# Kernel optimization log

Hardware: AMD Instinct MI355X
Metric: run time of the kernel (lower is better)

The kernel has to match this reference:

```python
import jax, jax.numpy as jnp
import numpy as np

DIM = 64  # per-head feature dim used for the 1/sqrt(dim) scale


def setup_inputs() -> dict:
    key = jax.random.key(0)
    kq, kk, kv, kw, kb = jax.random.split(key, 5)
    B, S, D, DK = 32, 4096, 64, 256
    q = jax.random.normal(kq, (B, S, D), dtype=jnp.float32)
    k = jax.random.normal(kk, (B, S, D), dtype=jnp.float32)
    v = jax.random.normal(kv, (B, S, D), dtype=jnp.float32)
    # Linear(input_size=S -> dim_k=DK): weight [DK, S], bias [DK]
    E_w = jax.random.normal(kw, (DK, S), dtype=jnp.float32) * (1.0 / np.sqrt(S))
    E_b = jax.random.normal(kb, (DK,), dtype=jnp.float32) * 0.01
    return {"q": q, "k": k, "v": v, "E_w": E_w, "E_b": E_b}


def reference(q, k, v, E_w, E_b):
    # K projection: k.transpose(1,2) -> [b, d, s]; E(k) -> [b, d, dim_k]
    K = jnp.einsum('bsd,ks->bdk', k, E_w) + E_b  # [b, d, dim_k]
    # scores = q @ K / sqrt(dim) -> [b, s, dim_k]
    scores = jnp.matmul(q, K) / jnp.sqrt(jnp.asarray(DIM, q.dtype))
    P_bar = jax.nn.softmax(scores, axis=-1)  # softmax over projected dim_k axis
    # V projection with F = E (parameter sharing): v -> [b, d, dim_k] -> transpose -> [b, dim_k, d]
    V = jnp.einsum('bsd,ks->bkd', v, E_w) + E_b[None, :, None]  # [b, dim_k, d]
    out = jnp.matmul(P_bar, V)  # [b, s, d]
    return out
```

## Files before the change

### kernel.cpp

```cpp
#include <hip/hip_runtime.h>
#include <hip/hip_bf16.h>
#include <stdint.h>

#define B_  32
#define S_  4096
#define D_  64
#define DK_ 256

typedef float f32x4 __attribute__((ext_vector_type(4)));
typedef short s16x8 __attribute__((ext_vector_type(8)));
typedef uint32_t u32x4 __attribute__((ext_vector_type(4)));

static __device__ __forceinline__ uint16_t f2bf(float f) {
    union { float f; uint32_t u; } x; x.f = f;
    uint32_t u = x.u;
    u += 0x7FFFu + ((u >> 16) & 1u);
    return (uint16_t)(u >> 16);
}

static __device__ __forceinline__ float bf2f(uint32_t hi16) {
    union { uint32_t u; float f; } x; x.u = hi16;
    return x.f;
}

static __device__ __forceinline__ uint32_t pk2(float a, float b) {
    __hip_bfloat162 h = __float22bfloat162_rn(float2{a, b});
    union { __hip_bfloat162 h; uint32_t u; } c; c.h = h;
    return c.u;
}

static __device__ __forceinline__ void gload_lds16(const uint16_t* g, uint16_t* l) {
    __builtin_amdgcn_global_load_lds(
        (const __attribute__((address_space(1))) uint32_t*)g,
        (__attribute__((address_space(3))) uint32_t*)l, 16, 0, 0);
}

__global__ __launch_bounds__(256) void ewcvt(const float* __restrict__ E_w,
                                             uint16_t* __restrict__ EwbS) {
    const int tg     = blockIdx.x * 256 + threadIdx.x;
    const int l16    = tg & 15;
    const int grp    = (tg >> 4) & 3;
    const int schunk = (tg >> 6) & 127;
    const int kktile = tg >> 13;
    const int kk = kktile*16 + l16;
    const int s  = schunk*32 + grp*8;
    const float4 f0 = *(const float4*)(E_w + (size_t)kk * S_ + s);
    const float4 f1 = *(const float4*)(E_w + (size_t)kk * S_ + s + 4);
    s16x8 o;
    o[0] = (short)f2bf(f0.x); o[1] = (short)f2bf(f0.y);
    o[2] = (short)f2bf(f0.z); o[3] = (short)f2bf(f0.w);
    o[4] = (short)f2bf(f1.x); o[5] = (short)f2bf(f1.y);
    o[6] = (short)f2bf(f1.z); o[7] = (short)f2bf(f1.w);
    *(s16x8*)(EwbS + (size_t)tg * 8) = o;
}

__global__ __launch_bounds__(256, 4) void proj_mfma(
        const uint16_t* __restrict__ EwbS,
        const float* __restrict__ kin, const float* __restrict__ vin,
        uint32_t* __restrict__ part) {
    const int bid = blockIdx.x;
    const int ss = bid & 15;
    const int b  = (bid >> 4) & 31;
    const int p  = bid >> 9;
    const float* x = (p ? vin : kin) + (size_t)b * S_ * D_;
    uint32_t* outp = part + ((size_t)((p*32 + b)*16 + ss)) * 8192;

    __shared__ __align__(16) uint16_t lds0[20 * 512];
    __shared__ __align__(16) uint16_t lds1[20 * 512];

    const int tid  = threadIdx.x;
    const int w    = tid >> 6;
    const int lane = tid & 63;
    const int l16  = lane & 15;
    const int grp  = lane >> 4;

    const uint16_t* srcA[4];
    #pragma unroll
    for (int i = 0; i < 4; ++i)
        srcA[i] = EwbS + ((((size_t)(w*4 + i))*128 + ss*8) << 9) + lane*8;

    const int dcol = tid & 63;
    const float* srcB = x + ((size_t)(ss*256 + w*8)) * D_ + dcol;
    const int boff = 16*512 + (dcol >> 4)*512 + (w*16 + (dcol & 15))*8;

    f32x4 acc[4][4] = {};

    {
        float xv[8];
        #pragma unroll
        for (int i = 0; i < 8; ++i) xv[i] = srcB[i * D_];
        #pragma unroll
        for (int i = 0; i < 4; ++i)
            gload_lds16(srcA[i], &lds0[(w*4 + i) * 512]);
        s16x8 h;
        #pragma unroll
        for (int i = 0; i < 8; ++i) h[i] = (short)f2bf(xv[i]);
        *(s16x8*)&lds0[boff] = h;
    }
    __syncthreads();

    #pragma unroll
    for (int t = 0; t < 8; ++t) {
        uint16_t* cur = (t & 1) ? lds1 : lds0;
        uint16_t* nxt = (t & 1) ? lds0 : lds1;

        float xv[8];
        if (t + 1 < 8) {
            const float* sB = srcB + (size_t)(t+1)*32*D_;
            #pragma unroll
            for (int i = 0; i < 8; ++i) xv[i] = sB[i * D_];
            #pragma unroll
            for (int i = 0; i < 4; ++i)
                gload_lds16(srcA[i] + (t+1)*512, &nxt[(w*4 + i) * 512]);
        }

        s16x8 bf[4];
        #pragma unroll
        for (int nt = 0; nt < 4; ++nt)
            bf[nt] = *(const s16x8*)&cur[(16 + nt) * 512 + lane*8];
        #pragma unroll
        for (int m = 0; m < 4; ++m) {
            const s16x8 af = *(const s16x8*)&cur[(w*4 + m) * 512 + lane*8];
            #pragma unroll
            for (int nt = 0; nt < 4; ++nt)
                acc[m][nt] = __builtin_amdgcn_mfma_f32_16x16x32_bf16(af, bf[nt], acc[m][nt], 0, 0, 0);
        }

        if (t + 1 < 8) {
            s16x8 h;
            #pragma unroll
            for (int i = 0; i < 8; ++i) h[i] = (short)f2bf(xv[i]);
            *(s16x8*)&nxt[boff] = h;
        }
        __syncthreads();
    }

    #pragma unroll
    for (int m = 0; m < 4; ++m) {
        const int kkrow = w*64 + m*16 + grp*4;
        #pragma unroll
        for (int nt = 0; nt < 4; ++nt) {
            const int didx = nt*16 + l16;
            outp[didx*128 + (kkrow >> 1)]     = pk2(acc[m][nt][0], acc[m][nt][1]);
            outp[didx*128 + (kkrow >> 1) + 1] = pk2(acc[m][nt][2], acc[m][nt][3]);
        }
    }
}

__global__ __launch_bounds__(256) void bias_reduce(
        const uint32_t* __restrict__ part, const float* __restrict__ E_b,
        uint16_t* __restrict__ Kbf, uint16_t* __restrict__ Vbf) {
    const int b  = blockIdx.x >> 2;
    const int dt = blockIdx.x & 3;
    const int t  = threadIdx.x;

    __shared__ uint16_t Kt[256][18];

    const uint32_t* Kp = part + ((size_t)(b*16))      * 8192 + dt*16*128;
    const uint32_t* Vp = part + ((size_t)((32+b)*16)) * 8192 + dt*16*128;

    #pragma unroll
    for (int j = 0; j < 8; ++j) {
        const int idx = j*256 + t;
        const int d_l = idx >> 7;
        const int kkp = idx & 127;
        float k0 = 0.f, k1 = 0.f, v0 = 0.f, v1 = 0.f;
        #pragma unroll
        for (int s = 0; s < 16; ++s) {
            const uint32_t ku = Kp[(size_t)s*8192 + d_l*128 + kkp];
            const uint32_t vu = Vp[(size_t)s*8192 + d_l*128 + kkp];
            k0 += bf2f(ku << 16);
            k1 += bf2f(ku & 0xffff0000u);
            v0 += bf2f(vu << 16);
            v1 += bf2f(vu & 0xffff0000u);
        }
        const int kk0 = kkp*2;
        const float b0 = E_b[kk0], b1 = E_b[kk0 + 1];
        *(uint32_t*)(Vbf + ((size_t)(b*64 + dt*16 + d_l))*256 + kk0) =
            (uint32_t)f2bf(v0 + b0) | ((uint32_t)f2bf(v1 + b1) << 16);
        Kt[kk0][d_l]     = f2bf(k0 + b0);
        Kt[kk0 + 1][d_l] = f2bf(k1 + b1);
    }
    __syncthreads();

    uint16_t* kout = Kbf + ((size_t)(b*256 + t))*64 + dt*16;
    s16x8 o0, o1;
    #pragma unroll
    for (int i = 0; i < 8; ++i) {
        o0[i] = (short)Kt[t][i];
        o1[i] = (short)Kt[t][8 + i];
    }
    *(s16x8*)kout       = o0;
    *(s16x8*)(kout + 8) = o1;
}

__global__ __launch_bounds__(512, 4) void attn(
        const float* __restrict__ q,
        const uint16_t* __restrict__ Kbf, const uint16_t* __restrict__ Vbf,
        float* __restrict__ out) {
    const int wg   = blockIdx.x;
    const int st   = wg & 31;
    const int b    = wg >> 5;
    const int tid  = threadIdx.x;
    const int wave = tid >> 6;
    const int lane = tid & 63;
    const int l16  = lane & 15;
    const int grp  = lane >> 4;
    const int s0   = st * 128 + wave * 16;

    __shared__ __align__(16) uint16_t Klds[16384];
    __shared__ __align__(16) uint16_t Vlds[16384];

    const uint16_t* Kb = Kbf + (size_t)b * DK_ * D_;
    const uint16_t* Vb = Vbf + (size_t)b * D_ * DK_;

    #pragma unroll
    for (int i = 0; i < 4; ++i) {
        const int s  = wave*4 + i;
        const int nt = s >> 1, kt = s & 1;
        gload_lds16(Kb + (size_t)(nt*16 + l16) * D_ + kt*32 + grp*8, &Klds[s*512]);
    }
    #pragma unroll
    for (int i = 0; i < 4; ++i) {
        const int s   = wave*4 + i;
        const int kt2 = s >> 2, nt2 = s & 3;
        gload_lds16(Vb + (size_t)(nt2*16 + l16) * DK_ + kt2*32 + grp*8, &Vlds[s*512]);
    }

    s16x8 qb[2];
    {
        const float* qp = q + ((size_t)b * S_ + s0 + l16) * D_;
        #pragma unroll
        for (int kt = 0; kt < 2; ++kt) {
            const int d0 = kt*32 + grp*8;
            const float4 f0 = *(const float4*)(qp + d0);
            const float4 f1 = *(const float4*)(qp + d0 + 4);
            s16x8 a;
            a[0] = (short)f2bf(f0.x * 0.125f);
            a[1] = (short)f2bf(f0.y * 0.125f);
            a[2] = (short)f2bf(f0.z * 0.125f);
            a[3] = (short)f2bf(f0.w * 0.125f);
            a[4] = (short)f2bf(f1.x * 0.125f);
            a[5] = (short)f2bf(f1.y * 0.125f);
            a[6] = (short)f2bf(f1.z * 0.125f);
            a[7] = (short)f2bf(f1.w * 0.125f);
            qb[kt] = a;
        }
    }

    __syncthreads();

    f32x4 acc[16] = {};
    #pragma unroll
    for (int nt = 0; nt < 16; ++nt) {
        #pragma unroll
        for (int kt = 0; kt < 2; ++kt) {
            const s16x8 kf = *(const s16x8*)&Klds[(nt*2 + kt)*512 + lane*8];
            acc[nt] = __builtin_amdgcn_mfma_f32_16x16x32_bf16(kf, qb[kt], acc[nt], 0, 0, 0);
        }
    }

    float sm = 0.f;
    #pragma unroll
    for (int nt = 0; nt < 16; ++nt) {
        #pragma unroll
        for (int r = 0; r < 4; ++r) {
            const float e = __expf(acc[nt][r]);
            acc[nt][r] = e;
            sm += e;
        }
    }
    sm += __shfl_xor(sm, 16);
    sm += __shfl_xor(sm, 32);
    const float inv = 1.f / sm;

    uint32_t pk[16][2];
    #pragma unroll
    for (int nt = 0; nt < 16; ++nt) {
        pk[nt][0] = pk2(acc[nt][0], acc[nt][1]);
        pk[nt][1] = pk2(acc[nt][2], acc[nt][3]);
    }

    float invs[4];
    #pragma unroll
    for (int r = 0; r < 4; ++r) invs[r] = __shfl(inv, grp*4 + r);

    const int sl0 = (((grp << 1) + 0) & 3) * 16 + l16;
    const int sl1 = (((grp << 1) + 1) & 3) * 16 + l16;
    const bool lohalf = (grp < 2);

    f32x4 o[4] = {};
    #pragma unroll
    for (int kt2 = 0; kt2 < 8; ++kt2) {
        union { u32x4 wv; s16x8 h; } u;
        #pragma unroll
        for (int c = 0; c < 4; ++c) {
            const int tt = c & 1;
            const int sl = (c >> 1) ? sl1 : sl0;
            const uint32_t lo = (uint32_t)__shfl((int)pk[2*kt2 + 0][tt], sl);
            const uint32_t hi = (uint32_t)__shfl((int)pk[2*kt2 + 1][tt], sl);
            u.wv[c] = lohalf ? lo : hi;
        }
        #pragma unroll
        for (int nt2 = 0; nt2 < 4; ++nt2) {
            const s16x8 vf = *(const s16x8*)&Vlds[(kt2*4 + nt2)*512 + lane*8];
            o[nt2] = __builtin_amdgcn_mfma_f32_16x16x32_bf16(u.h, vf, o[nt2], 0, 0, 0);
        }
    }

    #pragma unroll
    for (int nt2 = 0; nt2 < 4; ++nt2)
        #pragma unroll
        for (int r = 0; r < 4; ++r)
            out[((size_t)b * S_ + s0 + grp*4 + r) * D_ + nt2*16 + l16] =
                o[nt2][r] * invs[r];
}

extern "C" void kernel_launch(void* const* d_in, const int* in_sizes, int n_in,
                              void* d_out, int out_size, void* d_ws, size_t ws_size,
                              hipStream_t stream) {
    const float* q   = (const float*)d_in[0];
    const float* k   = (const float*)d_in[1];
    const float* v   = (const float*)d_in[2];
    const float* E_w = (const float*)d_in[3];
    const float* E_b = (const float*)d_in[4];
    float* out = (float*)d_out;

    char* ws = (char*)d_ws;
    uint32_t* part = (uint32_t*)(ws);
    uint16_t* Kbf  = (uint16_t*)(ws + (32u << 20));
    uint16_t* Vbf  = (uint16_t*)(ws + (33u << 20));
    uint16_t* EwbS = (uint16_t*)(ws + (34u << 20));

    ewcvt<<<512, 256, 0, stream>>>(E_w, EwbS);
    proj_mfma<<<1024, 256, 0, stream>>>(EwbS, k, v, part);
    bias_reduce<<<128, 256, 0, stream>>>(part, E_b, Kbf, Vbf);
    attn<<<1024, 512, 0, stream>>>(q, Kbf, Vbf, out);
}
```

Baseline: 64.82 us.

## Stage projection inputs once in LDS, read E_w fragments directly, split bias_reduce finer

proj_mfma now converts and stages all eight k/v sub-tiles into one LDS buffer up front, behind a single barrier. The E_w fragments are read straight from global memory instead of being async-copied into double-buffered LDS with a barrier every step. This drops the per-step synchronisation but loses overlap of global loads with MFMA, and each wave now reads its A fragments from global/L2. bias_reduce is split into 256 blocks of 8 d-columns instead of 128 blocks of 16, which gives more parallelism for the reduction.

```diff
diff --git a/kernel.cpp b/kernel.cpp
--- a/kernel.cpp
+++ b/kernel.cpp
@@ -65,8 +65,7 @@
     const float* x = (p ? vin : kin) + (size_t)b * S_ * D_;
     uint32_t* outp = part + ((size_t)((p*32 + b)*16 + ss)) * 8192;
 
-    __shared__ __align__(16) uint16_t lds0[20 * 512];
-    __shared__ __align__(16) uint16_t lds1[20 * 512];
+    __shared__ __align__(16) uint16_t Bx[32 * 512];
 
     const int tid  = threadIdx.x;
     const int w    = tid >> 6;
@@ -74,65 +73,39 @@
     const int l16  = lane & 15;
     const int grp  = lane >> 4;
 
-    const uint16_t* srcA[4];
-    #pragma unroll
-    for (int i = 0; i < 4; ++i)
-        srcA[i] = EwbS + ((((size_t)(w*4 + i))*128 + ss*8) << 9) + lane*8;
-
-    const int dcol = tid & 63;
-    const float* srcB = x + ((size_t)(ss*256 + w*8)) * D_ + dcol;
-    const int boff = 16*512 + (dcol >> 4)*512 + (w*16 + (dcol & 15))*8;
-
-    f32x4 acc[4][4] = {};
-
     {
-        float xv[8];
-        #pragma unroll
-        for (int i = 0; i < 8; ++i) xv[i] = srcB[i * D_];
-        #pragma unroll
-        for (int i = 0; i < 4; ++i)
-            gload_lds16(srcA[i], &lds0[(w*4 + i) * 512]);
-        s16x8 h;
-        #pragma unroll
-        for (int i = 0; i < 8; ++i) h[i] = (short)f2bf(xv[i]);
-        *(s16x8*)&lds0[boff] = h;
-    }
-    __syncthreads();
-
-    #pragma unroll
-    for (int t = 0; t < 8; ++t) {
-        uint16_t* cur = (t & 1) ? lds1 : lds0;
-        uint16_t* nxt = (t & 1) ? lds0 : lds1;
-
-        float xv[8];
-        if (t + 1 < 8) {
-            const float* sB = srcB + (size_t)(t+1)*32*D_;
+        const int dcol = tid & 63;
+        const float* srcB = x + ((size_t)(ss*256 + w*8)) * D_ + dcol;
+        const int boff0 = ((dcol >> 4) << 9) + ((w*16 + (dcol & 15)) << 3);
+        #pragma unroll
+        for (int ks = 0; ks < 8; ++ks) {
+            const float* sB = srcB + (size_t)ks*32*D_;
+            float xv[8];
             #pragma unroll
             for (int i = 0; i < 8; ++i) xv[i] = sB[i * D_];
+            s16x8 h;
             #pragma unroll
-            for (int i = 0; i < 4; ++i)
-                gload_lds16(srcA[i] + (t+1)*512, &nxt[(w*4 + i) * 512]);
-        }
-
+            for (int i = 0; i < 8; ++i) h[i] = (short)f2bf(xv[i]);
+            *(s16x8*)&Bx[(ks << 11) + boff0] = h;
+        }
+    }
+    __syncthreads();
+
+    const uint16_t* aBase = EwbS + ((size_t)(w*4)*128 + ss*8) * 512 + lane*8;
+    f32x4 acc[4][4] = {};
+    #pragma unroll
+    for (int ks = 0; ks < 8; ++ks) {
         s16x8 bf[4];
         #pragma unroll
         for (int nt = 0; nt < 4; ++nt)
-            bf[nt] = *(const s16x8*)&cur[(16 + nt) * 512 + lane*8];
+            bf[nt] = *(const s16x8*)&Bx[((ks*4 + nt) << 9) + lane*8];
         #pragma unroll
         for (int m = 0; m < 4; ++m) {
-            const s16x8 af = *(const s16x8*)&cur[(w*4 + m) * 512 + lane*8];
+            const s16x8 af = *(const s16x8*)(aBase + ((size_t)m*128 + ks) * 512);
             #pragma unroll
             for (int nt = 0; nt < 4; ++nt)
                 acc[m][nt] = __builtin_amdgcn_mfma_f32_16x16x32_bf16(af, bf[nt], acc[m][nt], 0, 0, 0);
         }
-
-        if (t + 1 < 8) {
-            s16x8 h;
-            #pragma unroll
-            for (int i = 0; i < 8; ++i) h[i] = (short)f2bf(xv[i]);
-            *(s16x8*)&nxt[boff] = h;
-        }
-        __syncthreads();
     }
 
     #pragma unroll
@@ -150,17 +123,17 @@
 __global__ __launch_bounds__(256) void bias_reduce(
         const uint32_t* __restrict__ part, const float* __restrict__ E_b,
         uint16_t* __restrict__ Kbf, uint16_t* __restrict__ Vbf) {
-    const int b  = blockIdx.x >> 2;
-    const int dt = blockIdx.x & 3;
+    const int b  = blockIdx.x >> 3;
+    const int dt = blockIdx.x & 7;
     const int t  = threadIdx.x;
 
-    __shared__ uint16_t Kt[256][18];
-
-    const uint32_t* Kp = part + ((size_t)(b*16))      * 8192 + dt*16*128;
-    const uint32_t* Vp = part + ((size_t)((32+b)*16)) * 8192 + dt*16*128;
-
-    #pragma unroll
-    for (int j = 0; j < 8; ++j) {
+    __shared__ uint16_t Kt[256][10];
+
+    const uint32_t* Kp = part + ((size_t)(b*16))      * 8192 + dt*8*128;
+    const uint32_t* Vp = part + ((size_t)((32+b)*16)) * 8192 + dt*8*128;
+
+    #pragma unroll
+    for (int j = 0; j < 4; ++j) {
         const int idx = j*256 + t;
         const int d_l = idx >> 7;
         const int kkp = idx & 127;
@@ -176,22 +149,18 @@
         }
         const int kk0 = kkp*2;
         const float b0 = E_b[kk0], b1 = E_b[kk0 + 1];
-        *(uint32_t*)(Vbf + ((size_t)(b*64 + dt*16 + d_l))*256 + kk0) =
+        *(uint32_t*)(Vbf + ((size_t)(b*64 + dt*8 + d_l))*256 + kk0) =
             (uint32_t)f2bf(v0 + b0) | ((uint32_t)f2bf(v1 + b1) << 16);
         Kt[kk0][d_l]     = f2bf(k0 + b0);
         Kt[kk0 + 1][d_l] = f2bf(k1 + b1);
     }
     __syncthreads();
 
-    uint16_t* kout = Kbf + ((size_t)(b*256 + t))*64 + dt*16;
-    s16x8 o0, o1;
-    #pragma unroll
-    for (int i = 0; i < 8; ++i) {
-        o0[i] = (short)Kt[t][i];
-        o1[i] = (short)Kt[t][8 + i];
-    }
-    *(s16x8*)kout       = o0;
-    *(s16x8*)(kout + 8) = o1;
+    uint16_t* kout = Kbf + ((size_t)(b*256 + t))*64 + dt*8;
+    s16x8 o0;
+    #pragma unroll
+    for (int i = 0; i < 8; ++i) o0[i] = (short)Kt[t][i];
+    *(s16x8*)kout = o0;
 }
 
 __global__ __launch_bounds__(512, 4) void attn(
@@ -334,6 +303,6 @@
 
     ewcvt<<<512, 256, 0, stream>>>(E_w, EwbS);
     proj_mfma<<<1024, 256, 0, stream>>>(EwbS, k, v, part);
-    bias_reduce<<<128, 256, 0, stream>>>(part, E_b, Kbf, Vbf);
+    bias_reduce<<<256, 256, 0, stream>>>(part, E_b, Kbf, Vbf);
     attn<<<1024, 512, 0, stream>>>(q, Kbf, Vbf, out);
 }
```

New measurement: 67.13 us. +3.6%, slower.
